# Kernel optimization log

Measured on AMD Instinct MI355X. Metric: run time of the kernel, lower is better.

## Reference

```python
import jax, jax.numpy as jnp
import numpy as np

B = 16      # batch (num jagged sequences)
N = 1024    # max seq length (mask size n)
D = 512     # embedding_dim
H = 8       # num_heads
DA = 64     # attention_dim per head
DV = 64     # linear_hidden_dim per head
EPS = 1e-6


def setup_inputs() -> dict:
    key = jax.random.key(0)
    k0, k1, k2, k3 = jax.random.split(key, 4)
    lengths = 512 + 16 * np.arange(B)            # deterministic jagged lengths, all <= N
    offsets = np.concatenate([[0], np.cumsum(lengths)]).astype(np.int64)  # (B+1,)
    T = int(offsets[-1])                          # 10112 total tokens
    x = jax.random.normal(k0, (T, D), jnp.float32)
    uvqk = jax.random.normal(k1, (D, 2 * H * DV + 2 * H * DA), jnp.float32) * 0.02
    # torch Linear weight is (out_features, in_features) = (D, H*DV), xavier-uniform scale
    lim = float(np.sqrt(6.0 / (D + H * DV)))
    o_weight = jax.random.uniform(k2, (D, H * DV), jnp.float32, -lim, lim)
    o_bias = jax.random.uniform(k3, (D,), jnp.float32, -0.01, 0.01)
    invalid_attn_mask = jnp.tril(jnp.ones((N, N), jnp.float32))  # causal {0,1} mask
    return {
        "x": x,
        "x_offsets": jnp.asarray(offsets),
        "invalid_attn_mask": invalid_attn_mask,
        "uvqk": uvqk,
        "o_weight": o_weight,
        "o_bias": o_bias,
    }


def _layer_norm(x):
    # F.layer_norm over last dim, no elementwise affine
    m = jnp.mean(x, axis=-1, keepdims=True)
    v = jnp.mean(jnp.square(x - m), axis=-1, keepdims=True)
    return (x - m) / jnp.sqrt(v + EPS)


def _jagged_to_padded(values, offsets, n):
    # values: (T, C) -> (B, n, C), zero padded
    lengths = offsets[1:] - offsets[:-1]               # (B,)
    pos = jnp.arange(n)                                # (n,)
    idx = offsets[:-1, None] + pos[None, :]            # (B, n)
    valid = pos[None, :] < lengths[:, None]            # (B, n)
    idx = jnp.where(valid, idx, 0)
    return values[idx] * valid[..., None].astype(values.dtype)


def _dense_to_jagged(padded, offsets, T):
    # padded: (B, n, C) -> (T, C)
    tok = jnp.arange(T)
    b = jnp.searchsorted(offsets, tok, side="right") - 1   # batch id per token
    p = tok - offsets[b]                                   # position within sequence
    return padded[b, p]


def reference(x, x_offsets, invalid_attn_mask, uvqk, o_weight, o_bias):
    T = x.shape[0]
    n = invalid_attn_mask.shape[-1]
    normed_x = _layer_norm(x)                              # (T, D)
    mm = jax.nn.silu(normed_x @ uvqk)                      # (T, 2*H*DV + 2*H*DA)
    u, v, q, k = jnp.split(mm, [H * DV, 2 * H * DV, 2 * H * DV + H * DA], axis=1)
    pq = _jagged_to_padded(q, x_offsets, n).reshape(-1, n, H, DA)  # (B,n,H,DA)
    pk = _jagged_to_padded(k, x_offsets, n).reshape(-1, n, H, DA)
    pv = _jagged_to_padded(v, x_offsets, n).reshape(-1, n, H, DV)
    qk = jnp.einsum("bqhd,bkhd->bhqk", pq, pk)             # (B,H,n,n)
    qk = (jax.nn.silu(qk) / n) * invalid_attn_mask[None, None]
    attn = jnp.einsum("bhqk,bkhd->bqhd", qk, pv).reshape(-1, n, H * DV)
    attn_j = _dense_to_jagged(attn, x_offsets, T)          # (T, H*DV)
    o_input = u * _layer_norm(attn_j)
    return o_input @ o_weight.T + o_bias + x
```

## Files before the change

### kernel.cpp

```cpp
#include <hip/hip_runtime.h>
#include <hip/hip_bf16.h>
#include <math.h>

typedef short bf16x8 __attribute__((ext_vector_type(8)));
typedef float f32x4 __attribute__((ext_vector_type(4)));

#define MFMA16x16(a, b, c) __builtin_amdgcn_mfma_f32_16x16x32_bf16(a, b, c, 0, 0, 0)

__device__ __forceinline__ float silu_f(float v) { return v / (1.0f + __expf(-v)); }
__device__ __forceinline__ int swz128(int b) { return b ^ (((b >> 7) & 7) << 4); }

__device__ __forceinline__ unsigned short f2bf(float f) {
  union { float f; unsigned u; } x; x.f = f;
  unsigned r = x.u + 0x7fffu + ((x.u >> 16) & 1u);
  return (unsigned short)(r >> 16);
}
__device__ __forceinline__ float bf2f(unsigned short h) {
  union { unsigned u; float f; } x; x.u = ((unsigned)h) << 16;
  return x.f;
}

__device__ __forceinline__ void gload_lds16(const void* g, void* l) {
  __builtin_amdgcn_global_load_lds((__attribute__((address_space(1))) unsigned int*)g,
                                   (__attribute__((address_space(3))) unsigned int*)l,
                                   16, 0, 0);
}

__global__ void k_prep_offs(const int* __restrict__ raw, int* __restrict__ offs, int Bp1) {
  int t = threadIdx.x;
  bool is64 = (raw[3] == 0);
  if (t < Bp1) offs[t] = is64 ? raw[2 * t] : raw[t];
}

__global__ __launch_bounds__(256) void k_conv_uvqkT(const float* __restrict__ uvqk,
                                                    unsigned short* __restrict__ uvqkT) {
  __shared__ float tile[32][33];
  int n0 = blockIdx.x * 32, k0 = blockIdx.y * 32;
  int tx = threadIdx.x & 31;
  int ty = threadIdx.x >> 5;
#pragma unroll
  for (int i = 0; i < 4; ++i)
    tile[ty + 8 * i][tx] = uvqk[(size_t)(k0 + ty + 8 * i) * 2048 + n0 + tx];
  __syncthreads();
#pragma unroll
  for (int i = 0; i < 4; ++i) {
    int nn = ty + 8 * i;
    uvqkT[(size_t)(n0 + nn) * 512 + k0 + tx] = f2bf(tile[tx][nn]);
  }
}

__global__ __launch_bounds__(256) void k_conv_bf16(const float* __restrict__ in,
                                                   unsigned short* __restrict__ out, int n) {
  int i = blockIdx.x * 256 + threadIdx.x;
  if (i < n) out[i] = f2bf(in[i]);
}

__global__ __launch_bounds__(256) void k_ln_x(const float* __restrict__ x,
                                              unsigned short* __restrict__ normed, int T) {
  int lane = threadIdx.x & 63, wid = threadIdx.x >> 6;
  int row = blockIdx.x * 4 + wid;
  if (row >= T) return;
  const float4* xr = (const float4*)(x + (size_t)row * 512);
  float4 a = xr[lane * 2], b = xr[lane * 2 + 1];
  float s = a.x + a.y + a.z + a.w + b.x + b.y + b.z + b.w;
  float s2 = a.x * a.x + a.y * a.y + a.z * a.z + a.w * a.w +
             b.x * b.x + b.y * b.y + b.z * b.z + b.w * b.w;
#pragma unroll
  for (int m = 1; m < 64; m <<= 1) { s += __shfl_xor(s, m); s2 += __shfl_xor(s2, m); }
  float mean = s * (1.0f / 512.0f);
  float var = s2 * (1.0f / 512.0f) - mean * mean;
  float rstd = rsqrtf(var + 1e-6f);
  float v[8] = {a.x, a.y, a.z, a.w, b.x, b.y, b.z, b.w};
  unsigned short o[8];
#pragma unroll
  for (int j = 0; j < 8; ++j) o[j] = f2bf((v[j] - mean) * rstd);
  *(uint4*)(normed + (size_t)row * 512 + lane * 8) = *(uint4*)o;
}

__global__ __launch_bounds__(256) void k_ln_mul_u(const float* __restrict__ attn,
                                                  const unsigned short* __restrict__ mm,
                                                  unsigned short* __restrict__ oin, int T) {
  int lane = threadIdx.x & 63, wid = threadIdx.x >> 6;
  int row = blockIdx.x * 4 + wid;
  if (row >= T) return;
  const float4* xr = (const float4*)(attn + (size_t)row * 512);
  float4 a = xr[lane * 2], b = xr[lane * 2 + 1];
  float s = a.x + a.y + a.z + a.w + b.x + b.y + b.z + b.w;
  float s2 = a.x * a.x + a.y * a.y + a.z * a.z + a.w * a.w +
             b.x * b.x + b.y * b.y + b.z * b.z + b.w * b.w;
#pragma unroll
  for (int m = 1; m < 64; m <<= 1) { s += __shfl_xor(s, m); s2 += __shfl_xor(s2, m); }
  float mean = s * (1.0f / 512.0f);
  float var = s2 * (1.0f / 512.0f) - mean * mean;
  float rstd = rsqrtf(var + 1e-6f);
  uint4 ub = *(const uint4*)(mm + (size_t)row * 2048 + lane * 8);
  const unsigned short* us = (const unsigned short*)&ub;
  float v[8] = {a.x, a.y, a.z, a.w, b.x, b.y, b.z, b.w};
  unsigned short o[8];
#pragma unroll
  for (int j = 0; j < 8; ++j) o[j] = f2bf((v[j] - mean) * rstd * bf2f(us[j]));
  *(uint4*)(oin + (size_t)row * 512 + lane * 8) = *(uint4*)o;
}

template <int MODE>
__global__ __launch_bounds__(256) void k_gemm_bt(const unsigned short* __restrict__ A,
                                                 const unsigned short* __restrict__ Bt,
                                                 void* __restrict__ Cout,
                                                 const float* __restrict__ bias,
                                                 const float* __restrict__ xres,
                                                 int M, int Nn, int K, int ntn) {
  __shared__ __align__(16) char lds[32768];
  char* ldsA = lds;
  char* ldsB = lds + 16384;
  int bid = blockIdx.x;
  int mt = bid / ntn, nt = bid - mt * ntn;
  int m0 = mt * 128, n0 = nt * 128;
  int tid = threadIdx.x, lane = tid & 63, wid = tid >> 6;
  int wm = wid >> 1, wn = wid & 1;
  int fr = lane & 15, fq = lane >> 4;
  f32x4 acc[4][4] = {};
  int nK = K >> 6;
  int lco = (lane & 7) * 16;
  int lrow8 = lane >> 3;
  for (int kt = 0; kt < nK; ++kt) {
    int k0 = kt << 6;
#pragma unroll
    for (int p = 0; p < 4; ++p) {
      int chunk = wid * 4 + p;
      int row = chunk * 8 + lrow8;
      int colb = lco ^ ((row & 7) << 4);
      int ar = m0 + row; if (ar >= M) ar = M - 1;
      gload_lds16((const char*)(A + (size_t)ar * K + k0) + colb, ldsA + chunk * 1024);
      gload_lds16((const char*)(Bt + (size_t)(n0 + row) * K + k0) + colb, ldsB + chunk * 1024);
    }
    __syncthreads();
    bf16x8 af[4][2], bfr[4][2];
#pragma unroll
    for (int mi = 0; mi < 4; ++mi) {
      int r = wm * 64 + mi * 16 + fr;
#pragma unroll
      for (int kk = 0; kk < 2; ++kk)
        af[mi][kk] = *(const bf16x8*)(ldsA + swz128(r * 128 + kk * 64 + fq * 16));
    }
#pragma unroll
    for (int ni = 0; ni < 4; ++ni) {
      int r = wn * 64 + ni * 16 + fr;
#pragma unroll
      for (int kk = 0; kk < 2; ++kk)
        bfr[ni][kk] = *(const bf16x8*)(ldsB + swz128(r * 128 + kk * 64 + fq * 16));
    }
#pragma unroll
    for (int mi = 0; mi < 4; ++mi)
#pragma unroll
      for (int ni = 0; ni < 4; ++ni) {
        acc[mi][ni] = MFMA16x16(af[mi][0], bfr[ni][0], acc[mi][ni]);
        acc[mi][ni] = MFMA16x16(af[mi][1], bfr[ni][1], acc[mi][ni]);
      }
    __syncthreads();
  }
#pragma unroll
  for (int mi = 0; mi < 4; ++mi) {
#pragma unroll
    for (int j = 0; j < 4; ++j) {
      int r = m0 + wm * 64 + mi * 16 + fq * 4 + j;
      if (r >= M) continue;
#pragma unroll
      for (int ni = 0; ni < 4; ++ni) {
        int c = n0 + wn * 64 + ni * 16 + fr;
        float v = acc[mi][ni][j];
        if (MODE == 0) {
          ((unsigned short*)Cout)[(size_t)r * Nn + c] = f2bf(silu_f(v));
        } else {
          ((float*)Cout)[(size_t)r * Nn + c] = v + bias[c] + xres[(size_t)r * 512 + c];
        }
      }
    }
  }
}

__global__ __launch_bounds__(256) void k_attn(const unsigned short* __restrict__ mm,
                                              const int* __restrict__ offs,
                                              float* __restrict__ attn, float inv_n) {
  int b = blockIdx.y >> 3, h = blockIdx.y & 7;
  int off = offs[b];
  int len = offs[b + 1] - off;
  int q0 = blockIdx.x * 64;
  if (q0 >= len) return;
  int tid = threadIdx.x, lane = tid & 63, wid = tid >> 6;
  int fr = lane & 15, fq = lane >> 4;
  __shared__ __align__(16) char sK[8192];
  __shared__ __align__(16) char sVT[8192];
  __shared__ __align__(16) char sP[8192];
  const unsigned short* qp = mm + (size_t)off * 2048 + 1024 + h * 64;
  const unsigned short* kp = mm + (size_t)off * 2048 + 1536 + h * 64;
  const unsigned short* vp = mm + (size_t)off * 2048 + 512 + h * 64;
  int qrow = q0 + wid * 16 + fr;
  int qrc = qrow < len ? qrow : len - 1;
  bf16x8 aq[2];
  aq[0] = *(const bf16x8*)(qp + (size_t)qrc * 2048 + fq * 8);
  aq[1] = *(const bf16x8*)(qp + (size_t)qrc * 2048 + 32 + fq * 8);
  f32x4 accO[4] = {};
  int nkt = (q0 >> 6) + 1;
  char* pw = sP + wid * 2048;
  for (int kt = 0; kt < nkt; ++kt) {
    int s0 = kt << 6;
    __syncthreads();
#pragma unroll 2
    for (int i = tid; i < 512; i += 256) {
      int row = i >> 3, cb = (i & 7) << 4;
      uint4 val = {0u, 0u, 0u, 0u};
      if (s0 + row < len) val = *(const uint4*)((const char*)(kp + (size_t)(s0 + row) * 2048) + cb);
      *(uint4*)(sK + swz128(row * 128 + cb)) = val;
    }
#pragma unroll 2
    for (int i = tid; i < 512; i += 256) {
      int s = i >> 3, d0 = (i & 7) << 3;
      uint4 val = {0u, 0u, 0u, 0u};
      if (s0 + s < len) val = *(const uint4*)((const char*)(vp + (size_t)(s0 + s) * 2048) + d0 * 2);
      const unsigned short* e = (const unsigned short*)&val;
#pragma unroll
      for (int j = 0; j < 8; ++j)
        *(unsigned short*)(sVT + swz128((d0 + j) * 128 + s * 2)) = e[j];
    }
    __syncthreads();
#pragma unroll
    for (int ni = 0; ni < 4; ++ni) {
      f32x4 sa = {};
      bf16x8 b0 = *(const bf16x8*)(sK + swz128((ni * 16 + fr) * 128 + fq * 16));
      bf16x8 b1 = *(const bf16x8*)(sK + swz128((ni * 16 + fr) * 128 + 64 + fq * 16));
      sa = MFMA16x16(aq[0], b0, sa);
      sa = MFMA16x16(aq[1], b1, sa);
#pragma unroll
      for (int j = 0; j < 4; ++j) {
        int pq = q0 + wid * 16 + fq * 4 + j;
        int ps = s0 + ni * 16 + fr;
        float v = (ps <= pq) ? silu_f(sa[j]) * inv_n : 0.0f;
        *(unsigned short*)(pw + swz128((fq * 4 + j) * 128 + (ni * 16 + fr) * 2)) = f2bf(v);
      }
    }
    bf16x8 pa0 = *(const bf16x8*)(pw + swz128(fr * 128 + fq * 16));
    bf16x8 pa1 = *(const bf16x8*)(pw + swz128(fr * 128 + 64 + fq * 16));
#pragma unroll
    for (int ni = 0; ni < 4; ++ni) {
      bf16x8 v0 = *(const bf16x8*)(sVT + swz128((ni * 16 + fr) * 128 + fq * 16));
      bf16x8 v1 = *(const bf16x8*)(sVT + swz128((ni * 16 + fr) * 128 + 64 + fq * 16));
      accO[ni] = MFMA16x16(pa0, v0, accO[ni]);
      accO[ni] = MFMA16x16(pa1, v1, accO[ni]);
    }
  }
#pragma unroll
  for (int ni = 0; ni < 4; ++ni)
#pragma unroll
    for (int j = 0; j < 4; ++j) {
      int pq = q0 + wid * 16 + fq * 4 + j;
      if (pq < len)
        attn[(size_t)(off + pq) * 512 + h * 64 + ni * 16 + fr] = accO[ni][j];
    }
}

extern "C" void kernel_launch(void* const* d_in, const int* in_sizes, int n_in,
                              void* d_out, int out_size, void* d_ws, size_t ws_size,
                              hipStream_t stream) {
  const float* x = (const float*)d_in[0];
  const int* xoff = (const int*)d_in[1];
  const float* uvqk = (const float*)d_in[3];
  const float* ow = (const float*)d_in[4];
  const float* obias = (const float*)d_in[5];

  const int D = 512;
  int T = in_sizes[0] / D;
  int B = in_sizes[1] - 1;
  int nm = 1;
  while ((long long)nm * nm < (long long)in_sizes[2]) nm <<= 1;

  char* w = (char*)d_ws;
  size_t p = 0;
  auto alloc = [&](size_t bytes) { size_t r = p; p += (bytes + 255) & ~(size_t)255; return r; };
  int* offs = (int*)(w + alloc(sizeof(int) * (size_t)(B + 1)));
  unsigned short* normed = (unsigned short*)(w + alloc((size_t)T * 512 * 2));
  unsigned short* mm = (unsigned short*)(w + alloc((size_t)T * 2048 * 2));
  float* attn = (float*)(w + alloc((size_t)T * 512 * 4));
  unsigned short* oin = (unsigned short*)(w + alloc((size_t)T * 512 * 2));
  unsigned short* uvqkT = (unsigned short*)(w + alloc((size_t)2048 * 512 * 2));
  unsigned short* owb = (unsigned short*)(w + alloc((size_t)512 * 512 * 2));

  k_prep_offs<<<1, 32, 0, stream>>>(xoff, offs, B + 1);
  k_conv_uvqkT<<<dim3(64, 16), 256, 0, stream>>>(uvqk, uvqkT);
  k_conv_bf16<<<1024, 256, 0, stream>>>(ow, owb, 512 * 512);
  k_ln_x<<<(T + 3) / 4, 256, 0, stream>>>(x, normed, T);
  int ntm = (T + 127) / 128;
  k_gemm_bt<0><<<ntm * 16, 256, 0, stream>>>(normed, uvqkT, (void*)mm, nullptr, nullptr,
                                             T, 2048, 512, 16);
  k_attn<<<dim3(nm / 64, B * 8), 256, 0, stream>>>(mm, offs, attn, 1.0f / (float)nm);
  k_ln_mul_u<<<(T + 3) / 4, 256, 0, stream>>>(attn, mm, oin, T);
  k_gemm_bt<1><<<ntm * 4, 256, 0, stream>>>(oin, owb, d_out, obias, x, T, 512, 512, 4);
}
```

Baseline: 239.4 us.

## Restructure attention as sync-free per-wave tiles with pre-transposed V

```diff
diff --git a/kernel.cpp b/kernel.cpp
--- a/kernel.cpp
+++ b/kernel.cpp
@@ -77,17 +77,20 @@
   *(uint4*)(normed + (size_t)row * 512 + lane * 8) = *(uint4*)o;
 }
 
-__global__ __launch_bounds__(256) void k_ln_mul_u(const float* __restrict__ attn,
+__global__ __launch_bounds__(256) void k_ln_mul_u(const unsigned short* __restrict__ attnb,
                                                   const unsigned short* __restrict__ mm,
                                                   unsigned short* __restrict__ oin, int T) {
   int lane = threadIdx.x & 63, wid = threadIdx.x >> 6;
   int row = blockIdx.x * 4 + wid;
   if (row >= T) return;
-  const float4* xr = (const float4*)(attn + (size_t)row * 512);
-  float4 a = xr[lane * 2], b = xr[lane * 2 + 1];
-  float s = a.x + a.y + a.z + a.w + b.x + b.y + b.z + b.w;
-  float s2 = a.x * a.x + a.y * a.y + a.z * a.z + a.w * a.w +
-             b.x * b.x + b.y * b.y + b.z * b.z + b.w * b.w;
+  uint4 av = *(const uint4*)(attnb + (size_t)row * 512 + lane * 8);
+  const unsigned short* ae = (const unsigned short*)&av;
+  float v[8];
+#pragma unroll
+  for (int j = 0; j < 8; ++j) v[j] = bf2f(ae[j]);
+  float s = 0.f, s2 = 0.f;
+#pragma unroll
+  for (int j = 0; j < 8; ++j) { s += v[j]; s2 += v[j] * v[j]; }
 #pragma unroll
   for (int m = 1; m < 64; m <<= 1) { s += __shfl_xor(s, m); s2 += __shfl_xor(s2, m); }
   float mean = s * (1.0f / 512.0f);
@@ -95,7 +98,6 @@
   float rstd = rsqrtf(var + 1e-6f);
   uint4 ub = *(const uint4*)(mm + (size_t)row * 2048 + lane * 8);
   const unsigned short* us = (const unsigned short*)&ub;
-  float v[8] = {a.x, a.y, a.z, a.w, b.x, b.y, b.z, b.w};
   unsigned short o[8];
 #pragma unroll
   for (int j = 0; j < 8; ++j) o[j] = f2bf((v[j] - mean) * rstd * bf2f(us[j]));
@@ -178,84 +180,108 @@
   }
 }
 
-__global__ __launch_bounds__(256) void k_attn(const unsigned short* __restrict__ mm,
-                                              const int* __restrict__ offs,
-                                              float* __restrict__ attn, float inv_n) {
-  int b = blockIdx.y >> 3, h = blockIdx.y & 7;
-  int off = offs[b];
-  int len = offs[b + 1] - off;
-  int q0 = blockIdx.x * 64;
-  if (q0 >= len) return;
+__global__ __launch_bounds__(256) void k_vT(const unsigned short* __restrict__ mm,
+                                            const int* __restrict__ offs,
+                                            unsigned short* __restrict__ vT) {
+  int bh = blockIdx.x; int b = bh >> 3, h = bh & 7;
+  int off = offs[b], len = offs[b + 1] - off;
+  int lane = threadIdx.x & 63, w = threadIdx.x >> 6;
+  const unsigned short* vp = mm + (size_t)off * 2048 + 512 + h * 64 + lane;
+  unsigned short* vt = vT + ((size_t)bh * 64 + lane) * 1024;
+  int nc = ((len + 63) & ~63) >> 3;
+  for (int c = w; c < nc; c += 4) {
+    int s8 = c << 3;
+    unsigned short r[8];
+#pragma unroll
+    for (int j = 0; j < 8; ++j)
+      r[j] = (s8 + j < len) ? vp[(size_t)(s8 + j) * 2048] : (unsigned short)0;
+    *(uint4*)(vt + s8) = *(uint4*)r;
+  }
+}
+
+__global__ __launch_bounds__(256) void k_attn2(const unsigned short* __restrict__ mm,
+                                               const unsigned short* __restrict__ vT,
+                                               const int* __restrict__ offs,
+                                               unsigned short* __restrict__ attnb,
+                                               float inv_n) {
+  __shared__ __align__(16) char sP[16384];
+  int bid = blockIdx.x;
+  int orig = (bid & 7) * 128 + (bid >> 3);
+  int bh = orig >> 3, grp = orig & 7;
+  int b = bh >> 3, h = bh & 7;
+  int off = offs[b], len = offs[b + 1] - off;
   int tid = threadIdx.x, lane = tid & 63, wid = tid >> 6;
+  int qb = grp * 128 + wid * 32;
+  if (qb >= len) return;
   int fr = lane & 15, fq = lane >> 4;
-  __shared__ __align__(16) char sK[8192];
-  __shared__ __align__(16) char sVT[8192];
-  __shared__ __align__(16) char sP[8192];
   const unsigned short* qp = mm + (size_t)off * 2048 + 1024 + h * 64;
   const unsigned short* kp = mm + (size_t)off * 2048 + 1536 + h * 64;
-  const unsigned short* vp = mm + (size_t)off * 2048 + 512 + h * 64;
-  int qrow = q0 + wid * 16 + fr;
-  int qrc = qrow < len ? qrow : len - 1;
-  bf16x8 aq[2];
-  aq[0] = *(const bf16x8*)(qp + (size_t)qrc * 2048 + fq * 8);
-  aq[1] = *(const bf16x8*)(qp + (size_t)qrc * 2048 + 32 + fq * 8);
-  f32x4 accO[4] = {};
-  int nkt = (q0 >> 6) + 1;
-  char* pw = sP + wid * 2048;
+  const unsigned short* vtp = vT + (size_t)bh * 64 * 1024;
+  bf16x8 aq[2][2];
+#pragma unroll
+  for (int mi = 0; mi < 2; ++mi) {
+    int qr = qb + mi * 16 + fr; if (qr >= len) qr = len - 1;
+#pragma unroll
+    for (int kk = 0; kk < 2; ++kk)
+      aq[mi][kk] = *(const bf16x8*)(qp + (size_t)qr * 2048 + kk * 32 + fq * 8);
+  }
+  f32x4 accO[2][4] = {};
+  char* pw = sP + wid * 4096;
+  int nkt = (qb >> 6) + 1;
   for (int kt = 0; kt < nkt; ++kt) {
     int s0 = kt << 6;
-    __syncthreads();
-#pragma unroll 2
-    for (int i = tid; i < 512; i += 256) {
-      int row = i >> 3, cb = (i & 7) << 4;
-      uint4 val = {0u, 0u, 0u, 0u};
-      if (s0 + row < len) val = *(const uint4*)((const char*)(kp + (size_t)(s0 + row) * 2048) + cb);
-      *(uint4*)(sK + swz128(row * 128 + cb)) = val;
-    }
-#pragma unroll 2
-    for (int i = tid; i < 512; i += 256) {
-      int s = i >> 3, d0 = (i & 7) << 3;
-      uint4 val = {0u, 0u, 0u, 0u};
-      if (s0 + s < len) val = *(const uint4*)((const char*)(vp + (size_t)(s0 + s) * 2048) + d0 * 2);
-      const unsigned short* e = (const unsigned short*)&val;
-#pragma unroll
-      for (int j = 0; j < 8; ++j)
-        *(unsigned short*)(sVT + swz128((d0 + j) * 128 + s * 2)) = e[j];
-    }
-    __syncthreads();
-#pragma unroll
-    for (int ni = 0; ni < 4; ++ni) {
-      f32x4 sa = {};
-      bf16x8 b0 = *(const bf16x8*)(sK + swz128((ni * 16 + fr) * 128 + fq * 16));
-      bf16x8 b1 = *(const bf16x8*)(sK + swz128((ni * 16 + fr) * 128 + 64 + fq * 16));
-      sa = MFMA16x16(aq[0], b0, sa);
-      sa = MFMA16x16(aq[1], b1, sa);
+    bf16x8 kf[4][2];
+#pragma unroll
+    for (int ni = 0; ni < 4; ++ni)
+#pragma unroll
+      for (int kk = 0; kk < 2; ++kk)
+        kf[ni][kk] = *(const bf16x8*)(kp + (size_t)(s0 + ni * 16 + fr) * 2048 + kk * 32 + fq * 8);
+#pragma unroll
+    for (int mi = 0; mi < 2; ++mi) {
+      f32x4 sacc[4] = {};
+#pragma unroll
+      for (int ni = 0; ni < 4; ++ni) {
+        sacc[ni] = MFMA16x16(aq[mi][0], kf[ni][0], sacc[ni]);
+        sacc[ni] = MFMA16x16(aq[mi][1], kf[ni][1], sacc[ni]);
+      }
+#pragma unroll
+      for (int ni = 0; ni < 4; ++ni)
+#pragma unroll
+        for (int j = 0; j < 4; ++j) {
+          int pq = qb + mi * 16 + fq * 4 + j;
+          int ps = s0 + ni * 16 + fr;
+          float v = (ps <= pq) ? silu_f(sacc[ni][j]) * inv_n : 0.0f;
+          *(unsigned short*)(pw + swz128((mi * 16 + fq * 4 + j) * 128 + (ni * 16 + fr) * 2)) =
+              f2bf(v);
+        }
+    }
+    bf16x8 vf[4][2];
+#pragma unroll
+    for (int nd = 0; nd < 4; ++nd)
+#pragma unroll
+      for (int kk = 0; kk < 2; ++kk)
+        vf[nd][kk] = *(const bf16x8*)(vtp + (size_t)(nd * 16 + fr) * 1024 + s0 + kk * 32 + fq * 8);
+#pragma unroll
+    for (int mi = 0; mi < 2; ++mi) {
+      bf16x8 pa0 = *(const bf16x8*)(pw + swz128((mi * 16 + fr) * 128 + fq * 16));
+      bf16x8 pa1 = *(const bf16x8*)(pw + swz128((mi * 16 + fr) * 128 + 64 + fq * 16));
+#pragma unroll
+      for (int nd = 0; nd < 4; ++nd) {
+        accO[mi][nd] = MFMA16x16(pa0, vf[nd][0], accO[mi][nd]);
+        accO[mi][nd] = MFMA16x16(pa1, vf[nd][1], accO[mi][nd]);
+      }
+    }
+  }
+#pragma unroll
+  for (int mi = 0; mi < 2; ++mi)
+#pragma unroll
+    for (int nd = 0; nd < 4; ++nd)
 #pragma unroll
       for (int j = 0; j < 4; ++j) {
-        int pq = q0 + wid * 16 + fq * 4 + j;
-        int ps = s0 + ni * 16 + fr;
-        float v = (ps <= pq) ? silu_f(sa[j]) * inv_n : 0.0f;
-        *(unsigned short*)(pw + swz128((fq * 4 + j) * 128 + (ni * 16 + fr) * 2)) = f2bf(v);
-      }
-    }
-    bf16x8 pa0 = *(const bf16x8*)(pw + swz128(fr * 128 + fq * 16));
-    bf16x8 pa1 = *(const bf16x8*)(pw + swz128(fr * 128 + 64 + fq * 16));
-#pragma unroll
-    for (int ni = 0; ni < 4; ++ni) {
-      bf16x8 v0 = *(const bf16x8*)(sVT + swz128((ni * 16 + fr) * 128 + fq * 16));
-      bf16x8 v1 = *(const bf16x8*)(sVT + swz128((ni * 16 + fr) * 128 + 64 + fq * 16));
-      accO[ni] = MFMA16x16(pa0, v0, accO[ni]);
-      accO[ni] = MFMA16x16(pa1, v1, accO[ni]);
-    }
-  }
-#pragma unroll
-  for (int ni = 0; ni < 4; ++ni)
-#pragma unroll
-    for (int j = 0; j < 4; ++j) {
-      int pq = q0 + wid * 16 + fq * 4 + j;
-      if (pq < len)
-        attn[(size_t)(off + pq) * 512 + h * 64 + ni * 16 + fr] = accO[ni][j];
-    }
+        int pq = qb + mi * 16 + fq * 4 + j;
+        if (pq < len)
+          attnb[(size_t)(off + pq) * 512 + h * 64 + nd * 16 + fr] = f2bf(accO[mi][nd][j]);
+      }
 }
 
 extern "C" void kernel_launch(void* const* d_in, const int* in_sizes, int n_in,
@@ -279,10 +305,11 @@
   int* offs = (int*)(w + alloc(sizeof(int) * (size_t)(B + 1)));
   unsigned short* normed = (unsigned short*)(w + alloc((size_t)T * 512 * 2));
   unsigned short* mm = (unsigned short*)(w + alloc((size_t)T * 2048 * 2));
-  float* attn = (float*)(w + alloc((size_t)T * 512 * 4));
+  unsigned short* attnb = (unsigned short*)(w + alloc((size_t)T * 512 * 2));
   unsigned short* oin = (unsigned short*)(w + alloc((size_t)T * 512 * 2));
   unsigned short* uvqkT = (unsigned short*)(w + alloc((size_t)2048 * 512 * 2));
   unsigned short* owb = (unsigned short*)(w + alloc((size_t)512 * 512 * 2));
+  unsigned short* vT = (unsigned short*)(w + alloc((size_t)B * 8 * 64 * (size_t)nm * 2));
 
   k_prep_offs<<<1, 32, 0, stream>>>(xoff, offs, B + 1);
   k_conv_uvqkT<<<dim3(64, 16), 256, 0, stream>>>(uvqk, uvqkT);
@@ -291,7 +318,8 @@
   int ntm = (T + 127) / 128;
   k_gemm_bt<0><<<ntm * 16, 256, 0, stream>>>(normed, uvqkT, (void*)mm, nullptr, nullptr,
                                              T, 2048, 512, 16);
-  k_attn<<<dim3(nm / 64, B * 8), 256, 0, stream>>>(mm, offs, attn, 1.0f / (float)nm);
-  k_ln_mul_u<<<(T + 3) / 4, 256, 0, stream>>>(attn, mm, oin, T);
+  k_vT<<<B * 8, 256, 0, stream>>>(mm, offs, vT);
+  k_attn2<<<(B * 8 * nm / 128), 256, 0, stream>>>(mm, vT, offs, attnb, 1.0f / (float)nm);
+  k_ln_mul_u<<<(T + 3) / 4, 256, 0, stream>>>(attnb, mm, oin, T);
   k_gemm_bt<1><<<ntm * 4, 256, 0, stream>>>(oin, owb, d_out, obias, x, T, 512, 512, 4);
 }
```

Measured after the change: 261.8 us. 1.09x slower.
